# Kernel optimization log

Measured on AMD Instinct MI355X. Metric: run time of the kernel, lower is better.

Reference implementation:

```python
import jax, jax.numpy as jnp
import numpy as np

DILATIONS = (48, 76, 96, 111, 124, 135, 144, 152)


def setup_inputs() -> dict:
    key = jax.random.key(0)
    kx, kw, kb = jax.random.split(key, 3)
    B_, C_IN, H, Wd = 8, 64, 128, 512
    C_OUT = 64
    x = jax.random.normal(kx, (B_, C_IN, H, Wd), dtype=jnp.float32)
    # stacked weights for 8 parallel branches: [branch, out_ch, in_ch, kh=1, kw=3]
    W = jax.random.normal(kw, (8, C_OUT, C_IN, 1, 3), dtype=jnp.float32) * 0.05
    B = jax.random.normal(kb, (8, C_OUT), dtype=jnp.float32) * 0.05
    return {"x": x, "W": W, "B": B}


def _dilated_conv(x, w, d):
    # 'same' padding for kernel (1,3) with dilation (1,d): pad d on each side of width
    return jax.lax.conv_general_dilated(
        x, w,
        window_strides=(1, 1),
        padding=[(0, 0), (d, d)],
        rhs_dilation=(1, d),
        dimension_numbers=("NCHW", "OIHW", "NCHW"),
    )


def reference(x, W, B):
    out = None
    for i, d in enumerate(DILATIONS):  # fixed small structural loop over branches
        y = _dilated_conv(x, W[i], d) + B[i][None, :, None, None]
        out = y if out is None else out + y
    return jax.nn.relu(out)
```

## Files before the change

### kernel.cpp

```cpp
#include <hip/hip_runtime.h>
#include <hip/hip_bf16.h>
#include <stdint.h>

typedef float  f32x4 __attribute__((ext_vector_type(4)));
typedef short  s16x8 __attribute__((ext_vector_type(8)));

#define NB    8
#define CIN   64
#define COUT  64
#define HH    128
#define WW    512
#define NTAP  17
#define PADW  152
#define XROW  816
#define BUFB  (XROW * 64)
#define HW    (HH * WW)

__global__ __launch_bounds__(256) void prep_wfrag(
        const float* __restrict__ W, const float* __restrict__ Bv,
        __hip_bfloat16* __restrict__ wf, float* __restrict__ bsum) {
    int idx = blockIdx.x * 256 + threadIdx.x;
    if (idx < NTAP * 2 * 4 * 64 * 8) {
        int j  = idx & 7;
        int l  = (idx >> 3) & 63;
        int m  = (idx >> 9) & 3;
        int pp = (idx >> 11) & 1;
        int t  = idx >> 12;
        int ci = pp * 32 + 8 * (l >> 4) + j;
        int co = 16 * m + (l & 15);
        float v;
        if (t == 0) {
            v = 0.f;
            #pragma unroll
            for (int i = 0; i < NB; ++i) v += W[((i * COUT + co) * CIN + ci) * 3 + 1];
        } else if (t <= 8) {
            v = W[(((t - 1) * COUT + co) * CIN + ci) * 3 + 0];
        } else {
            v = W[(((t - 9) * COUT + co) * CIN + ci) * 3 + 2];
        }
        wf[idx] = __float2bfloat16(v);
    }
    if (idx < COUT) {
        float s = 0.f;
        #pragma unroll
        for (int i = 0; i < NB; ++i) s += Bv[i * COUT + idx];
        bsum[idx] = s;
    }
}

static constexpr int OFFS[NTAP] = {0, -48, -76, -96, -111, -124, -135, -144, -152,
                                      48,  76,  96,  111,  124,  135,  144,  152};

#define SB __builtin_amdgcn_sched_barrier(0)

#define LOADAF(AF, T0, CNT)                                                    \
    _Pragma("unroll")                                                          \
    for (int i = 0; i < (CNT); ++i)                                            \
        _Pragma("unroll")                                                      \
        for (int mm = 0; mm < 2; ++mm)                                         \
            AF[i][mm] = *reinterpret_cast<const s16x8*>(                       \
                wbase + ((T0) + i) * 8192 + (2 * mg + mm) * 1024);

#define COMPTAPS(AF, T0, CNT)                                                  \
    _Pragma("unroll")                                                          \
    for (int i = 0; i < (CNT); ++i) {                                          \
        const int t      = (T0) + i;                                           \
        const int ldsrow = rowb + OFFS[t];                                     \
        const int slot   = lhi ^ ((ldsrow >> 1) & 3);                          \
        const char* bbase = rb + ldsrow * 64 + slot * 16;                      \
        s16x8 bfr[8];                                                          \
        _Pragma("unroll")                                                      \
        for (int n = 0; n < 8; ++n)                                            \
            bfr[n] = *reinterpret_cast<const s16x8*>(bbase + n * 1024);        \
        _Pragma("unroll")                                                      \
        for (int mm = 0; mm < 2; ++mm)                                         \
            _Pragma("unroll")                                                  \
            for (int n = 0; n < 8; ++n)                                        \
                acc[mm][n] = __builtin_amdgcn_mfma_f32_16x16x32_bf16(          \
                    AF[i][mm], bfr[n], acc[mm][n], 0, 0, 0);                   \
    }

#define UNIT_SCHED(U, B1,C1, B2,C2, B3,C3, B4,C4, B5,C5, B6,C6)                \
    {                                                                          \
        s16x8 afA[3][2], afB[3][2];                                            \
        LOADAF(afA, B1, C1)   SB;                                              \
        LOADAF(afB, B2, C2)   SB;                                              \
        if ((U) < 7) SLOAD((U) + 1);                                           \
        SB;                                                                    \
        COMPTAPS(afA, B1, C1) SB;                                              \
        LOADAF(afA, B3, C3)   SB;                                              \
        COMPTAPS(afB, B2, C2) SB;                                              \
        LOADAF(afB, B4, C4)   SB;                                              \
        COMPTAPS(afA, B3, C3) SB;                                              \
        LOADAF(afA, B5, C5)   SB;                                              \
        COMPTAPS(afB, B4, C4) SB;                                              \
        LOADAF(afB, B6, C6)   SB;                                              \
        COMPTAPS(afA, B5, C5) SB;                                              \
        COMPTAPS(afB, B6, C6) SB;                                              \
    }

__global__ __launch_bounds__(512, 2) void hdc_mfma(
        const float* __restrict__ x, const __hip_bfloat16* __restrict__ wf,
        const float* __restrict__ bsum, float* __restrict__ out) {
    extern __shared__ __align__(16) char smem[];

    const int tid  = threadIdx.x;
    const int wv   = tid >> 6;
    const int lane = tid & 63;
    const int l15  = lane & 15;
    const int lhi  = lane >> 4;
    const int mg   = wv >> 2;
    const int ws   = wv & 3;
    const int c    = tid >> 7;
    const int wl   = tid & 127;
    const int bh0  = blockIdx.x * 4;
    const int wlo  = ws * 128;
    const int rowb = PADW + wlo + l15;

    f32x4 acc[2][8];
    #pragma unroll
    for (int mm = 0; mm < 2; ++mm) {
        f32x4 bi = *reinterpret_cast<const f32x4*>(
            bsum + mg * 32 + 16 * mm + 4 * lhi);
        #pragma unroll
        for (int n = 0; n < 8; ++n) acc[mm][n] = bi;
    }

    {
        const int4 z{0, 0, 0, 0};
        #pragma unroll
        for (int bb = 0; bb < 2; ++bb) {
            int4* base = reinterpret_cast<int4*>(smem + bb * BUFB);
            for (int f = tid; f < 608; f += 512) {
                base[f] = z;
                base[2656 + f] = z;
            }
        }
    }

    float4 xv[8];

    auto SLOAD = [&](int u) {
        const int r = bh0 + (u >> 1);
        const int b = r >> 7, h = r & 127;
        const float* src = x +
            (((size_t)(b * CIN + (u & 1) * 32 + c * 8) * HH + h) * WW) + wl * 4;
        #pragma unroll
        for (int j = 0; j < 8; ++j)
            xv[j] = *reinterpret_cast<const float4*>(src + j * HW);
    };
    auto SWRITE = [&](int u) {
        char* dst = smem + (u & 1) * BUFB;
        #pragma unroll
        for (int k = 0; k < 4; ++k) {
            const int row  = PADW + wl * 4 + k;
            const int slot = c ^ ((row >> 1) & 3);
            union { __hip_bfloat16 hs[8]; int4 iv; } pk;
            #pragma unroll
            for (int j = 0; j < 8; ++j)
                pk.hs[j] = __float2bfloat16(((const float*)&xv[j])[k]);
            *reinterpret_cast<int4*>(dst + row * 64 + slot * 16) = pk.iv;
        }
    };

    SLOAD(0);
    asm volatile("s_waitcnt vmcnt(0)" ::: "memory");
    SB;
    SWRITE(0);
    __syncthreads();

    for (int u = 0; u < 8; ++u) {
        const char* wbase = (const char*)wf + (u & 1) * 4096 + lane * 16;
        const char* rb    = smem + (u & 1) * BUFB;

        if (mg == 0) {
            UNIT_SCHED(u, 0,3, 3,3, 6,3, 9,3, 12,3, 15,2)
        } else {
            UNIT_SCHED(u, 9,3, 12,3, 15,2, 0,3, 3,3, 6,3)
        }

        if (u & 1) {
            const int r = bh0 + (u >> 1);
            const int b = r >> 7, h = r & 127;
            float* obase = out +
                (((size_t)b * COUT + mg * 32 + 4 * lhi) * HH + h) * WW + wlo + l15;
            #pragma unroll
            for (int mm = 0; mm < 2; ++mm)
                #pragma unroll
                for (int n = 0; n < 8; ++n)
                    #pragma unroll
                    for (int rr = 0; rr < 4; ++rr) {
                        float v = acc[mm][n][rr];
                        obase[(size_t)(16 * mm + rr) * HW + 16 * n] =
                            v > 0.f ? v : 0.f;
                    }
            #pragma unroll
            for (int mm = 0; mm < 2; ++mm) {
                f32x4 bi = *reinterpret_cast<const f32x4*>(
                    bsum + mg * 32 + 16 * mm + 4 * lhi);
                #pragma unroll
                for (int n = 0; n < 8; ++n) acc[mm][n] = bi;
            }
        }

        if (u < 7) {
            asm volatile("s_waitcnt vmcnt(0)" ::: "memory");
            SB;
            SWRITE(u + 1);
        }

        asm volatile("s_waitcnt lgkmcnt(0)" ::: "memory");
        SB;
        __builtin_amdgcn_s_barrier();
    }
}

#define CI_STAGE 16

__global__ void prep_weff_fb(const float* __restrict__ W, const float* __restrict__ Bv,
                             float* __restrict__ weff, float* __restrict__ bsum) {
    int idx = blockIdx.x * 256 + threadIdx.x;
    if (idx < CIN * NTAP * COUT) {
        int co = idx & 63;
        int t  = (idx >> 6) % NTAP;
        int ci = idx / (NTAP * COUT);
        float v;
        if (t == 0) {
            v = 0.f;
            #pragma unroll
            for (int i = 0; i < NB; ++i) v += W[(((i * COUT + co) * CIN + ci) * 3) + 1];
        } else if (t <= 8) {
            v = W[((((t - 1) * COUT + co) * CIN + ci) * 3) + 0];
        } else {
            v = W[((((t - 9) * COUT + co) * CIN + ci) * 3) + 2];
        }
        weff[(ci * NTAP + t) * COUT + co] = v;
    }
    if (idx < COUT) {
        float s = 0.f;
        #pragma unroll
        for (int i = 0; i < NB; ++i) s += Bv[i * COUT + idx];
        bsum[idx] = s;
    }
}

__global__ __launch_bounds__(256, 2) void hdc_fb(
        const float* __restrict__ x, const float* __restrict__ weff,
        const float* __restrict__ bsum, float* __restrict__ out) {
    __shared__ float xsf[CI_STAGE][XROW];
    const int bh  = blockIdx.x;
    const int b   = bh >> 7;
    const int h   = bh & (HH - 1);
    const int tid = threadIdx.x;
    const int cg  = tid >> 5;
    const int wl  = tid & 31;
    float acc[8][16];
    #pragma unroll
    for (int j = 0; j < 8; ++j) {
        const float bj = bsum[cg * 8 + j];
        #pragma unroll
        for (int i = 0; i < 16; ++i) acc[j][i] = bj;
    }
    const float* xrowbase = x + ((size_t)(b * CIN) * HH + h) * WW;
    for (int s = 0; s < CIN / CI_STAGE; ++s) {
        __syncthreads();
        for (int f = tid; f < CI_STAGE * PADW; f += 256) {
            int r = f / PADW, cc = f - r * PADW;
            xsf[r][cc] = 0.f;
            xsf[r][PADW + WW + cc] = 0.f;
        }
        #pragma unroll
        for (int j = 0; j < 8; ++j) {
            int flat = j * 256 + tid;
            int r = flat >> 7, c4 = flat & 127;
            const float4 v = *reinterpret_cast<const float4*>(
                xrowbase + (size_t)(s * CI_STAGE + r) * HW + c4 * 4);
            *reinterpret_cast<float4*>(&xsf[r][PADW + c4 * 4]) = v;
        }
        __syncthreads();
        for (int r = 0; r < CI_STAGE; ++r) {
            const int ci = s * CI_STAGE + r;
            const float* wrow = weff + (size_t)(ci * NTAP) * COUT + cg * 8;
            const float* xr   = &xsf[r][PADW + wl];
            #pragma unroll
            for (int t = 0; t < NTAP; ++t) {
                const float4 w0 = *reinterpret_cast<const float4*>(wrow + t * COUT);
                const float4 w1 = *reinterpret_cast<const float4*>(wrow + t * COUT + 4);
                float xvv[16];
                #pragma unroll
                for (int i = 0; i < 16; ++i) xvv[i] = xr[OFFS[t] + 32 * i];
                const float wv2[8] = {w0.x, w0.y, w0.z, w0.w, w1.x, w1.y, w1.z, w1.w};
                #pragma unroll
                for (int j = 0; j < 8; ++j)
                    #pragma unroll
                    for (int i = 0; i < 16; ++i)
                        acc[j][i] = fmaf(wv2[j], xvv[i], acc[j][i]);
            }
        }
    }
    float* outbase = out + (((size_t)b * COUT + cg * 8) * HH + h) * WW + wl;
    #pragma unroll
    for (int j = 0; j < 8; ++j)
        #pragma unroll
        for (int i = 0; i < 16; ++i) {
            float v = acc[j][i];
            outbase[(size_t)j * HW + 32 * i] = v > 0.f ? v : 0.f;
        }
}


extern "C" void kernel_launch(void* const* d_in, const int* in_sizes, int n_in,
                              void* d_out, int out_size, void* d_ws, size_t ws_size,
                              hipStream_t stream) {
    const float* x  = (const float*)d_in[0];
    const float* W  = (const float*)d_in[1];
    const float* Bv = (const float*)d_in[2];
    float* out = (float*)d_out;

    const size_t need = 139264 + 256;

    if (ws_size >= need) {
        __hip_bfloat16* wf = (__hip_bfloat16*)d_ws;
        float* bsum = (float*)((char*)d_ws + 139264);
        prep_wfrag<<<272, 256, 0, stream>>>(W, Bv, wf, bsum);
        (void)hipFuncSetAttribute((const void*)hdc_mfma,
            hipFuncAttributeMaxDynamicSharedMemorySize, 2 * BUFB);
        hdc_mfma<<<256, 512, 2 * BUFB, stream>>>(x, wf, bsum, out);
    } else {
        float* weff = (float*)d_ws;
        float* bsum = weff + (size_t)CIN * NTAP * COUT;
        prep_weff_fb<<<(CIN * NTAP * COUT + 255) / 256, 256, 0, stream>>>(W, Bv, weff, bsum);
        hdc_fb<<<NB * HH, 256, 0, stream>>>(x, weff, bsum, out);
    }
}
```

Before: 78.77 us.

## Split each output row into half-width blocks with single-buffered staging

The persistent 256-block kernel, which looped over four rows per block with double-buffered LDS and prefetching, is replaced by 2048 blocks of 256 threads. Each block computes half of one output row. It stages a 560-column padded window per input-channel half into a single static LDS buffer and zero-fills out-of-range columns from global memory instead of pre-zeroing. This raises block count and occupancy (3 blocks per CU with smaller LDS) and removes the cross-iteration pipeline. In exchange it loses load/compute overlap inside a block and re-reads the halo columns that the two half-row blocks share.

```diff
diff --git a/kernel.cpp b/kernel.cpp
--- a/kernel.cpp
+++ b/kernel.cpp
@@ -12,8 +12,8 @@
 #define WW    512
 #define NTAP  17
 #define PADW  152
-#define XROW  816
-#define BUFB  (XROW * 64)
+#define WSPAN 256
+#define BROWS (WSPAN + 2 * PADW)
 #define HW    (HH * WW)
 
 __global__ __launch_bounds__(256) void prep_wfrag(
@@ -67,7 +67,7 @@
         const int t      = (T0) + i;                                           \
         const int ldsrow = rowb + OFFS[t];                                     \
         const int slot   = lhi ^ ((ldsrow >> 1) & 3);                          \
-        const char* bbase = rb + ldsrow * 64 + slot * 16;                      \
+        const char* bbase = smem + ldsrow * 64 + slot * 16;                    \
         s16x8 bfr[8];                                                          \
         _Pragma("unroll")                                                      \
         for (int n = 0; n < 8; ++n)                                            \
@@ -80,13 +80,11 @@
                     AF[i][mm], bfr[n], acc[mm][n], 0, 0, 0);                   \
     }
 
-#define UNIT_SCHED(U, B1,C1, B2,C2, B3,C3, B4,C4, B5,C5, B6,C6)                \
+#define PHASE_SCHED(B1,C1, B2,C2, B3,C3, B4,C4, B5,C5, B6,C6)                  \
     {                                                                          \
         s16x8 afA[3][2], afB[3][2];                                            \
         LOADAF(afA, B1, C1)   SB;                                              \
         LOADAF(afB, B2, C2)   SB;                                              \
-        if ((U) < 7) SLOAD((U) + 1);                                           \
-        SB;                                                                    \
         COMPTAPS(afA, B1, C1) SB;                                              \
         LOADAF(afA, B3, C3)   SB;                                              \
         COMPTAPS(afB, B2, C2) SB;                                              \
@@ -99,21 +97,24 @@
         COMPTAPS(afB, B6, C6) SB;                                              \
     }
 
-__global__ __launch_bounds__(512, 2) void hdc_mfma(
+__global__ __launch_bounds__(256, 3) void hdc_mfma(
         const float* __restrict__ x, const __hip_bfloat16* __restrict__ wf,
         const float* __restrict__ bsum, float* __restrict__ out) {
-    extern __shared__ __align__(16) char smem[];
+    __shared__ __align__(16) char smem[BROWS * 64];
 
     const int tid  = threadIdx.x;
     const int wv   = tid >> 6;
     const int lane = tid & 63;
     const int l15  = lane & 15;
     const int lhi  = lane >> 4;
-    const int mg   = wv >> 2;
-    const int ws   = wv & 3;
-    const int c    = tid >> 7;
-    const int wl   = tid & 127;
-    const int bh0  = blockIdx.x * 4;
+    const int mg   = wv >> 1;
+    const int ws   = wv & 1;
+    const int c    = tid >> 6;
+    const int wl   = tid & 63;
+    const int bid  = blockIdx.x;
+    const int row  = bid >> 1;
+    const int wh   = bid & 1;
+    const int b    = row >> 7, h = row & 127;
     const int wlo  = ws * 128;
     const int rowb = PADW + wlo + l15;
 
@@ -126,96 +127,67 @@
         for (int n = 0; n < 8; ++n) acc[mm][n] = bi;
     }
 
-    {
-        const int4 z{0, 0, 0, 0};
-        #pragma unroll
-        for (int bb = 0; bb < 2; ++bb) {
-            int4* base = reinterpret_cast<int4*>(smem + bb * BUFB);
-            for (int f = tid; f < 608; f += 512) {
-                base[f] = z;
-                base[2656 + f] = z;
+    auto STAGE = [&](int p) {
+        #pragma unroll
+        for (int q = 0; q < 3; ++q) {
+            const int r0 = q * 256 + wl * 4;
+            if (r0 < BROWS) {
+                const int gw = wh * WSPAN + r0 - PADW;
+                const bool in = (gw >= 0) && (gw < WW);
+                const float* src = x +
+                    (((size_t)(b * CIN + p * 32 + c * 8) * HH + h) * WW);
+                float4 xv[8];
+                #pragma unroll
+                for (int j = 0; j < 8; ++j) {
+                    float4 v{0.f, 0.f, 0.f, 0.f};
+                    if (in) v = *reinterpret_cast<const float4*>(
+                                    src + (size_t)j * HW + gw);
+                    xv[j] = v;
+                }
+                #pragma unroll
+                for (int k = 0; k < 4; ++k) {
+                    const int r    = r0 + k;
+                    const int slot = c ^ ((r >> 1) & 3);
+                    union { __hip_bfloat16 hs[8]; int4 iv; } pk;
+                    #pragma unroll
+                    for (int j = 0; j < 8; ++j)
+                        pk.hs[j] = __float2bfloat16(((const float*)&xv[j])[k]);
+                    *reinterpret_cast<int4*>(smem + r * 64 + slot * 16) = pk.iv;
+                }
             }
         }
-    }
-
-    float4 xv[8];
-
-    auto SLOAD = [&](int u) {
-        const int r = bh0 + (u >> 1);
-        const int b = r >> 7, h = r & 127;
-        const float* src = x +
-            (((size_t)(b * CIN + (u & 1) * 32 + c * 8) * HH + h) * WW) + wl * 4;
-        #pragma unroll
-        for (int j = 0; j < 8; ++j)
-            xv[j] = *reinterpret_cast<const float4*>(src + j * HW);
     };
-    auto SWRITE = [&](int u) {
-        char* dst = smem + (u & 1) * BUFB;
-        #pragma unroll
-        for (int k = 0; k < 4; ++k) {
-            const int row  = PADW + wl * 4 + k;
-            const int slot = c ^ ((row >> 1) & 3);
-            union { __hip_bfloat16 hs[8]; int4 iv; } pk;
+
+    #pragma unroll
+    for (int p = 0; p < 2; ++p) {
+        if (p) __syncthreads();
+        STAGE(p);
+        __syncthreads();
+
+        const char* wbase = (const char*)wf + p * 4096 + lane * 16;
+        if (mg == 0) {
+            PHASE_SCHED(0,3, 3,3, 6,3, 9,3, 12,3, 15,2)
+        } else {
+            PHASE_SCHED(9,3, 12,3, 15,2, 0,3, 3,3, 6,3)
+        }
+    }
+
+    float* obase = out +
+        (((size_t)b * COUT + mg * 32 + 4 * lhi) * HH + h) * WW +
+        wh * WSPAN + wlo + l15;
+    #pragma unroll
+    for (int mm = 0; mm < 2; ++mm)
+        #pragma unroll
+        for (int n = 0; n < 8; ++n)
             #pragma unroll
-            for (int j = 0; j < 8; ++j)
-                pk.hs[j] = __float2bfloat16(((const float*)&xv[j])[k]);
-            *reinterpret_cast<int4*>(dst + row * 64 + slot * 16) = pk.iv;
-        }
-    };
-
-    SLOAD(0);
-    asm volatile("s_waitcnt vmcnt(0)" ::: "memory");
-    SB;
-    SWRITE(0);
-    __syncthreads();
-
-    for (int u = 0; u < 8; ++u) {
-        const char* wbase = (const char*)wf + (u & 1) * 4096 + lane * 16;
-        const char* rb    = smem + (u & 1) * BUFB;
-
-        if (mg == 0) {
-            UNIT_SCHED(u, 0,3, 3,3, 6,3, 9,3, 12,3, 15,2)
-        } else {
-            UNIT_SCHED(u, 9,3, 12,3, 15,2, 0,3, 3,3, 6,3)
-        }
-
-        if (u & 1) {
-            const int r = bh0 + (u >> 1);
-            const int b = r >> 7, h = r & 127;
-            float* obase = out +
-                (((size_t)b * COUT + mg * 32 + 4 * lhi) * HH + h) * WW + wlo + l15;
-            #pragma unroll
-            for (int mm = 0; mm < 2; ++mm)
-                #pragma unroll
-                for (int n = 0; n < 8; ++n)
-                    #pragma unroll
-                    for (int rr = 0; rr < 4; ++rr) {
-                        float v = acc[mm][n][rr];
-                        obase[(size_t)(16 * mm + rr) * HW + 16 * n] =
-                            v > 0.f ? v : 0.f;
-                    }
-            #pragma unroll
-            for (int mm = 0; mm < 2; ++mm) {
-                f32x4 bi = *reinterpret_cast<const f32x4*>(
-                    bsum + mg * 32 + 16 * mm + 4 * lhi);
-                #pragma unroll
-                for (int n = 0; n < 8; ++n) acc[mm][n] = bi;
+            for (int rr = 0; rr < 4; ++rr) {
+                float v = acc[mm][n][rr];
+                obase[(size_t)(16 * mm + rr) * HW + 16 * n] = v > 0.f ? v : 0.f;
             }
-        }
-
-        if (u < 7) {
-            asm volatile("s_waitcnt vmcnt(0)" ::: "memory");
-            SB;
-            SWRITE(u + 1);
-        }
-
-        asm volatile("s_waitcnt lgkmcnt(0)" ::: "memory");
-        SB;
-        __builtin_amdgcn_s_barrier();
-    }
 }
 
 #define CI_STAGE 16
+#define XROW 816
 
 __global__ void prep_weff_fb(const float* __restrict__ W, const float* __restrict__ Bv,
                              float* __restrict__ weff, float* __restrict__ bsum) {
@@ -323,9 +295,7 @@
         __hip_bfloat16* wf = (__hip_bfloat16*)d_ws;
         float* bsum = (float*)((char*)d_ws + 139264);
         prep_wfrag<<<272, 256, 0, stream>>>(W, Bv, wf, bsum);
-        (void)hipFuncSetAttribute((const void*)hdc_mfma,
-            hipFuncAttributeMaxDynamicSharedMemorySize, 2 * BUFB);
-        hdc_mfma<<<256, 512, 2 * BUFB, stream>>>(x, wf, bsum, out);
+        hdc_mfma<<<2048, 256, 0, stream>>>(x, wf, bsum, out);
     } else {
         float* weff = (float*)d_ws;
         float* bsum = weff + (size_t)CIN * NTAP * COUT;
```

Measured after the change: 123.9 us. 1.57x slower.
